# Kernel optimization log

Measured on AMD Instinct MI355X. Metric: run time of the kernel, lower is better.

Reference implementation:

```python
import math
import jax, jax.numpy as jnp
import numpy as np

NUM_HEADS = 12
HEAD_DIM = 64
HIDDEN = NUM_HEADS * HEAD_DIM  # 768
SEQ = 4096


def setup_inputs() -> dict:
    key = jax.random.key(0)
    ks = jax.random.split(key, 7)
    s = 0.02  # BERT-style init scale for weights
    return {
        "hidden_states": jax.random.normal(ks[0], (1, SEQ, HIDDEN), jnp.float32),
        "Wq": jax.random.normal(ks[1], (HIDDEN, HIDDEN), jnp.float32) * s,
        "bq": jax.random.normal(ks[2], (HIDDEN,), jnp.float32) * s,
        "Wk": jax.random.normal(ks[3], (HIDDEN, HIDDEN), jnp.float32) * s,
        "bk": jax.random.normal(ks[4], (HIDDEN,), jnp.float32) * s,
        "Wv": jax.random.normal(ks[5], (HIDDEN, HIDDEN), jnp.float32) * s,
        "bv": jax.random.normal(ks[6], (HIDDEN,), jnp.float32) * s,
    }


def _split_heads(z):
    # [S, HIDDEN] -> [H, S, dh]
    S = z.shape[0]
    return jnp.transpose(z.reshape(S, NUM_HEADS, HEAD_DIM), (1, 0, 2))


def reference(hidden_states, Wq, bq, Wk, bk, Wv, bv):
    # batch is squeezed in the original module (kernel is unbatched)
    x = hidden_states[0]  # [S, D]
    q = _split_heads(x @ Wq.T + bq)  # [H, S, dh]
    k = _split_heads(x @ Wk.T + bk)  # [H, S, dh]
    scale = 1.0 / math.sqrt(HEAD_DIM)
    scores = jnp.einsum('hqd,hkd->hqk', q, k) * scale  # [H, S, S]
    probs = jax.nn.softmax(scores, axis=-1)
    # multi_rand_attn_cuda approximates P @ (x @ Wv^T + bv) via CDF-driven
    # Monte-Carlo column sampling of Wv; its expectation is the exact product,
    # which is the correctness baseline computed here.
    v = _split_heads(x @ Wv.T + bv)  # [H, S, dh]
    ctx = jnp.einsum('hqk,hkd->hqd', probs, v)  # [H, S, dh]
    ctx = jnp.transpose(ctx, (1, 0, 2)).reshape(x.shape[0], HIDDEN)
    return ctx[None]  # [1, S, D]
```

## Files before the change

### kernel.cpp

```cpp
#include <hip/hip_runtime.h>
#include <stdint.h>


typedef float    f32x4 __attribute__((ext_vector_type(4)));
typedef _Float16 h16x8 __attribute__((ext_vector_type(8)));
typedef _Float16 h16x4 __attribute__((ext_vector_type(4)));
typedef _Float16 h16x2 __attribute__((ext_vector_type(2)));
typedef __fp16   fp16x2 __attribute__((ext_vector_type(2)));
typedef unsigned short u16;

#define MFMA32(A, B, C) __builtin_amdgcn_mfma_f32_16x16x32_f16((A), (B), (C), 0, 0, 0)
#define ZERO4 ((f32x4){0.f, 0.f, 0.f, 0.f})

#define SEQ 4096
#define HID 768
#define NH  12
#define DH  64

#define CEXP 0.18033688011112042f

__device__ __forceinline__ u16 f2h(float f) {
  union { _Float16 h; u16 u; } v;
  v.h = (_Float16)f;
  return v.u;
}
__device__ __forceinline__ float h2f(u16 u) {
  union { u16 u; _Float16 h; } v;
  v.u = u;
  return (float)v.h;
}

__device__ __forceinline__ void gload_lds16(const void* g, void* l) {
  __builtin_amdgcn_global_load_lds(
      (__attribute__((address_space(1))) void*)(g),
      (__attribute__((address_space(3))) void*)(l),
      16, 0, 0);
}

__global__ __launch_bounds__(256) void cast_all_k(
    const float* __restrict__ x,  const float* __restrict__ wq,
    const float* __restrict__ wk, const float* __restrict__ wv,
    u16* __restrict__ xh,  u16* __restrict__ wqh,
    u16* __restrict__ wkh, u16* __restrict__ wvh)
{
  int i = blockIdx.x * 256 + threadIdx.x;
  const int NX4 = (SEQ * HID) / 4;
  const int NW4 = (HID * HID) / 4;
  const float4* src; ushort4* dst; int idx;
  if (i < NX4) {
    src = (const float4*)x; dst = (ushort4*)xh; idx = i;
  } else {
    int j = i - NX4;
    int w = j / NW4;
    idx = j - w * NW4;
    src = (const float4*)(w == 0 ? wq : (w == 1 ? wk : wv));
    dst = (ushort4*)(w == 0 ? wqh : (w == 1 ? wkh : wvh));
  }
  float4 v = src[idx];
  ushort4 o;
  o.x = f2h(v.x); o.y = f2h(v.y); o.z = f2h(v.z); o.w = f2h(v.w);
  dst[idx] = o;
}

__global__ __launch_bounds__(256, 3) void qkv_gemm_k(
    const u16* __restrict__ xh,
    const u16* __restrict__ wqh, const u16* __restrict__ wkh, const u16* __restrict__ wvh,
    const float* __restrict__ bq, const float* __restrict__ bk, const float* __restrict__ bv,
    u16* __restrict__ Qh, u16* __restrict__ Kh, u16* __restrict__ Vt)
{
  __shared__ u16 S[128 * 128];

  const int t = threadIdx.x;
  const int wave = t >> 6, lane = t & 63;
  const int m = lane & 15, quad = lane >> 4;
  const int z  = blockIdx.z;
  const int n0 = blockIdx.x * 128;
  const int m0 = blockIdx.y * 128;

  const u16*   W    = (z == 0) ? wqh : (z == 1) ? wkh : wvh;
  const float* bias = (z == 0) ? bq  : (z == 1) ? bk  : bv;

  const int wm = (wave >> 1) * 64;
  const int wn = (wave & 1) * 64;

  f32x4 acc[4][4];
#pragma unroll
  for (int i = 0; i < 4; i++)
#pragma unroll
    for (int j = 0; j < 4; j++) acc[i][j] = ZERO4;

  const int srow = wave * 8 + (lane >> 3);
  const int scg  = (lane & 7) ^ (srow & 7);
  const u16* gA = xh + (m0 + srow) * HID + scg * 8;
  const u16* gB = W  + (n0 + srow) * HID + scg * 8;
  u16* lA = S + wave * 512;
  u16* lB = S + 8192 + wave * 512;

  for (int k0 = 0; k0 < HID; k0 += 64) {
    __syncthreads();
#pragma unroll
    for (int c = 0; c < 4; c++) {
      gload_lds16(gA + c * 32 * HID + k0, lA + c * 2048);
      gload_lds16(gB + c * 32 * HID + k0, lB + c * 2048);
    }
    __syncthreads();

#pragma unroll
    for (int s = 0; s < 2; s++) {
      h16x8 af[4], bf[4];
#pragma unroll
      for (int i = 0; i < 4; i++)
        af[i] = *(const h16x8*)(S + (wm + i * 16 + m) * 64
                                + ((s * 4 + quad) ^ (m & 7)) * 8);
#pragma unroll
      for (int j = 0; j < 4; j++)
        bf[j] = *(const h16x8*)(S + 8192 + (wn + j * 16 + m) * 64
                                + ((s * 4 + quad) ^ (m & 7)) * 8);
#pragma unroll
      for (int i = 0; i < 4; i++)
#pragma unroll
        for (int j = 0; j < 4; j++)
          acc[i][j] = MFMA32(af[i], bf[j], acc[i][j]);
    }
  }

  __syncthreads();

  if (z < 2) {
    const float sc = (z == 0) ? CEXP : 1.0f;
#pragma unroll
    for (int i = 0; i < 4; i++) {
      int sl = wm + i * 16 + quad * 4;
#pragma unroll
      for (int j = 0; j < 4; j++) {
        int colp = wn + j * 16 + m;
        float bb = bias[n0 + colp];
        int c = colp >> 3, sub = colp & 7;
#pragma unroll
        for (int r = 0; r < 4; r++)
          S[(sl + r) * 128 + ((c ^ ((sl + r) & 15)) * 8) + sub] =
              f2h((acc[i][j][r] + bb) * sc);
      }
    }
    __syncthreads();
    u16* outp = (z == 0) ? Qh : Kh;
    const int ch = t & 15;
#pragma unroll
    for (int rr = 0; rr < 8; rr++) {
      int s = rr * 16 + (t >> 4);
      h16x8 v = *(const h16x8*)(S + s * 128 + ((ch ^ (s & 15)) * 8));
      *(h16x8*)(outp + (m0 + s) * HID + n0 + ch * 8) = v;
    }
  } else {
#pragma unroll
    for (int i = 0; i < 4; i++) {
      int sl = wm + i * 16 + quad * 4;
      int vp = (sl & ~31) + ((sl >> 2) & 3) * 8 + ((sl >> 4) & 1) * 4;
#pragma unroll
      for (int j = 0; j < 4; j++) {
        int nl = wn + j * 16 + m;
        float bb = bias[n0 + nl];
        h16x4 o;
        o[0] = (_Float16)(acc[i][j][0] + bb);
        o[1] = (_Float16)(acc[i][j][1] + bb);
        o[2] = (_Float16)(acc[i][j][2] + bb);
        o[3] = (_Float16)(acc[i][j][3] + bb);
        *(h16x4*)(S + nl * 128 + (((vp >> 3) ^ (nl & 15)) * 8) + (vp & 7)) = o;
      }
    }
    __syncthreads();
    const int ch = t & 15;
#pragma unroll
    for (int rr = 0; rr < 8; rr++) {
      int n = rr * 16 + (t >> 4);
      h16x8 v = *(const h16x8*)(S + n * 128 + ((ch ^ (n & 15)) * 8));
      *(h16x8*)(Vt + (n0 + n) * SEQ + m0 + ch * 8) = v;
    }
  }
}

__global__ __launch_bounds__(256, 3) void attn_k(
    const u16* __restrict__ Qh, const u16* __restrict__ Kh, const u16* __restrict__ Vt,
    float* __restrict__ out0, u16* __restrict__ Op1, float* __restrict__ Lp)
{
  __shared__ u16 Ks[128 * 64];
  __shared__ u16 Vs[64 * 128];

  const int t = threadIdx.x;
  const int wave = t >> 6, lane = t & 63;
  const int m = lane & 15, quad = lane >> 4;
  const int h  = blockIdx.y;
  const int q0 = blockIdx.x * 128;
  const int sp = blockIdx.z;
  const int kvbase = sp * 2048;

  h16x8 qf[2][2];
#pragma unroll
  for (int qn = 0; qn < 2; qn++)
#pragma unroll
    for (int ks = 0; ks < 2; ks++)
      qf[qn][ks] = *(const h16x8*)(Qh + (q0 + wave * 32 + qn * 16 + m) * HID
                                   + h * DH + ks * 32 + quad * 8);

  f32x4 O[2][4];
#pragma unroll
  for (int qn = 0; qn < 2; qn++)
#pragma unroll
    for (int jd = 0; jd < 4; jd++) O[qn][jd] = ZERO4;
  float lsum[2] = {0.f, 0.f};

  const int krow_b = wave * 8 + (lane >> 3);
  const int kcl    = lane & 7;
  const int vrow_b = wave * 4 + (lane >> 4);
  const int vcl    = lane & 15;

  for (int it = 0; it < 16; ++it) {
    const int kv0 = kvbase + it * 128;
    __syncthreads();
#pragma unroll
    for (int c = 0; c < 4; c++) {
      int row = c * 32 + krow_b;
      int cg  = kcl ^ (row & 7);
      gload_lds16(Kh + (kv0 + row) * HID + h * DH + cg * 8,
                  Ks + c * 2048 + wave * 512);
      int d  = c * 16 + vrow_b;
      int vg = vcl ^ (d & 15);
      gload_lds16(Vt + (h * DH + d) * SEQ + kv0 + vg * 8,
                  Vs + c * 2048 + wave * 512);
    }
    __syncthreads();

#pragma unroll
    for (int p = 0; p < 4; ++p) {
      const int krow0 = (2 * p) * 16 + m;
      const int krow1 = krow0 + 16;
      h16x8 kb00 = *(const h16x8*)(Ks + krow0 * 64 + ((    quad) ^ (m & 7)) * 8);
      h16x8 kb01 = *(const h16x8*)(Ks + krow0 * 64 + ((4 + quad) ^ (m & 7)) * 8);
      h16x8 kb10 = *(const h16x8*)(Ks + krow1 * 64 + ((    quad) ^ (m & 7)) * 8);
      h16x8 kb11 = *(const h16x8*)(Ks + krow1 * 64 + ((4 + quad) ^ (m & 7)) * 8);

      h16x8 vb[4];
#pragma unroll
      for (int jd = 0; jd < 4; jd++) {
        int d = jd * 16 + m;
        vb[jd] = *(const h16x8*)(Vs + d * 128 + (((p * 4 + quad) ^ m) * 8));
      }

#pragma unroll
      for (int qn = 0; qn < 2; qn++) {
        f32x4 S0 = MFMA32(kb00, qf[qn][0], ZERO4);
        S0       = MFMA32(kb01, qf[qn][1], S0);
        f32x4 S1 = MFMA32(kb10, qf[qn][0], ZERO4);
        S1       = MFMA32(kb11, qf[qn][1], S1);

        float e0 = __builtin_amdgcn_exp2f(S0[0]);
        float e1 = __builtin_amdgcn_exp2f(S0[1]);
        float e2 = __builtin_amdgcn_exp2f(S0[2]);
        float e3 = __builtin_amdgcn_exp2f(S0[3]);
        float e4 = __builtin_amdgcn_exp2f(S1[0]);
        float e5 = __builtin_amdgcn_exp2f(S1[1]);
        float e6 = __builtin_amdgcn_exp2f(S1[2]);
        float e7 = __builtin_amdgcn_exp2f(S1[3]);
        lsum[qn] += ((e0 + e1) + (e2 + e3)) + ((e4 + e5) + (e6 + e7));

        fp16x2 p01 = __builtin_amdgcn_cvt_pkrtz(e0, e1);
        fp16x2 p23 = __builtin_amdgcn_cvt_pkrtz(e2, e3);
        fp16x2 p45 = __builtin_amdgcn_cvt_pkrtz(e4, e5);
        fp16x2 p67 = __builtin_amdgcn_cvt_pkrtz(e6, e7);
        h16x2 q01 = __builtin_bit_cast(h16x2, p01);
        h16x2 q23 = __builtin_bit_cast(h16x2, p23);
        h16x2 q45 = __builtin_bit_cast(h16x2, p45);
        h16x2 q67 = __builtin_bit_cast(h16x2, p67);
        h16x4 pl = __builtin_shufflevector(q01, q23, 0, 1, 2, 3);
        h16x4 ph = __builtin_shufflevector(q45, q67, 0, 1, 2, 3);
        h16x8 pa = __builtin_shufflevector(pl, ph, 0, 1, 2, 3, 4, 5, 6, 7);

#pragma unroll
        for (int jd = 0; jd < 4; jd++)
          O[qn][jd] = MFMA32(pa, vb[jd], O[qn][jd]);
      }
    }
  }

#pragma unroll
  for (int qn = 0; qn < 2; qn++) {
    float v = lsum[qn];
    v += __shfl_xor(v, 16, 64);
    v += __shfl_xor(v, 32, 64);
    if (quad == 0)
      Lp[sp * NH * SEQ + h * SEQ + q0 + wave * 32 + qn * 16 + m] = v;
#pragma unroll
    for (int jd = 0; jd < 4; jd++) {
      int col = h * DH + jd * 16 + m;
#pragma unroll
      for (int r = 0; r < 4; r++) {
        int row = q0 + wave * 32 + qn * 16 + quad * 4 + r;
        if (sp == 0) out0[row * HID + col] = O[qn][jd][r];
        else         Op1[row * HID + col] = f2h(O[qn][jd][r]);
      }
    }
  }
}

__global__ __launch_bounds__(256) void reduce_k(
    float* __restrict__ out, const u16* __restrict__ Op1,
    const float* __restrict__ Lp)
{
  int i = blockIdx.x * 256 + threadIdx.x;
  int s  = i / 192;
  int c4 = i - s * 192;
  int h  = c4 >> 4;
  float L = Lp[h * SEQ + s] + Lp[NH * SEQ + h * SEQ + s];
  float inv = __builtin_amdgcn_rcpf(L);
  float4 a = ((const float4*)out)[i];
  ushort4 b = ((const ushort4*)Op1)[i];
  float4 r;
  r.x = (a.x + h2f(b.x)) * inv;
  r.y = (a.y + h2f(b.y)) * inv;
  r.z = (a.z + h2f(b.z)) * inv;
  r.w = (a.w + h2f(b.w)) * inv;
  ((float4*)out)[i] = r;
}

extern "C" void kernel_launch(void* const* d_in, const int* in_sizes, int n_in,
                              void* d_out, int out_size, void* d_ws, size_t ws_size,
                              hipStream_t stream) {
  const float* x  = (const float*)d_in[0];
  const float* Wq = (const float*)d_in[1];
  const float* bq = (const float*)d_in[2];
  const float* Wk = (const float*)d_in[3];
  const float* bk = (const float*)d_in[4];
  const float* Wv = (const float*)d_in[5];
  const float* bv = (const float*)d_in[6];
  float* out = (float*)d_out;

  char* ws = (char*)d_ws;
  u16* Qh  = (u16*)(ws);
  u16* Kh  = (u16*)(ws + 6291456);
  u16* Vt  = (u16*)(ws + 12582912);
  u16* xh  = (u16*)(ws + 18874368);
  u16* wqh = (u16*)(ws + 25165824);
  u16* wkh = (u16*)(ws + 26345472);
  u16* wvh = (u16*)(ws + 27525120);
  u16*   Op1 = (u16*)(ws + 18874368);
  float* Lp  = (float*)(ws + 25165824);

  cast_all_k<<<4800, 256, 0, stream>>>(x, Wq, Wk, Wv, xh, wqh, wkh, wvh);
  qkv_gemm_k<<<dim3(6, 32, 3), 256, 0, stream>>>(xh, wqh, wkh, wvh,
                                                 bq, bk, bv, Qh, Kh, Vt);
  attn_k<<<dim3(32, NH, 2), 256, 0, stream>>>(Qh, Kh, Vt, out, Op1, Lp);
  reduce_k<<<3072, 256, 0, stream>>>(out, Op1, Lp);
}
```

Baseline: 160.6 us.

## Double-buffer K/V tiles in attention and compute row sums via MFMA

Changes the attention inner loop from single-buffered 128-key tiles with two syncthreads per iteration to double-buffered 64-key tiles. The next tile's global-to-LDS load is issued before computing on the current one, with explicit vmcnt waits and raw barriers. The softmax denominator is now computed with an extra MFMA against a ones vector instead of VALU adds and shuffles, and MFMA sections get raised wave priority. This aims to hide load latency and cut VALU work, at the cost of an extra MFMA per step and hand-managed waitcnt correctness.

New measurement: 159.2 us. About the same (-0.8%).

```diff
diff --git a/kernel.cpp b/kernel.cpp
--- a/kernel.cpp
+++ b/kernel.cpp
@@ -18,6 +18,8 @@
 #define DH  64
 
 #define CEXP 0.18033688011112042f
+
+#define WAITV(N) asm volatile("s_waitcnt vmcnt(" #N ")" ::: "memory")
 
 __device__ __forceinline__ u16 f2h(float f) {
   union { _Float16 h; u16 u; } v;
@@ -179,12 +181,84 @@
   }
 }
 
+
+__device__ __forceinline__ void stage_kv(const u16* gKb, const u16* gVb,
+                                         u16* lK, u16* lV, int kv0)
+{
+#pragma unroll
+  for (int c = 0; c < 2; c++) {
+    gload_lds16(gKb + (kv0 + c * 32) * HID, lK + c * 2048);
+    gload_lds16(gVb + c * 32 * SEQ + kv0,   lV + c * 2048);
+  }
+}
+
+__device__ __forceinline__ void attn_compute(
+    const u16* __restrict__ Kb, const u16* __restrict__ Vb,
+    const h16x8 (&qf)[2][2], f32x4 (&O)[2][4], f32x4 (&Lacc)[2],
+    h16x8 onesv, int m, int quad)
+{
+#pragma unroll
+  for (int p = 0; p < 2; ++p) {
+    const int krow0 = 32 * p + m;
+    const int krow1 = krow0 + 16;
+    h16x8 kb00 = *(const h16x8*)(Kb + krow0 * 64 + ((    quad) ^ (m & 7)) * 8);
+    h16x8 kb01 = *(const h16x8*)(Kb + krow0 * 64 + ((4 + quad) ^ (m & 7)) * 8);
+    h16x8 kb10 = *(const h16x8*)(Kb + krow1 * 64 + ((    quad) ^ (m & 7)) * 8);
+    h16x8 kb11 = *(const h16x8*)(Kb + krow1 * 64 + ((4 + quad) ^ (m & 7)) * 8);
+
+    h16x8 vb[4];
+#pragma unroll
+    for (int jd = 0; jd < 4; jd++) {
+      int d = jd * 16 + m;
+      vb[jd] = *(const h16x8*)(Vb + d * 64 + (((p * 4 + quad) ^ (m & 7)) * 8));
+    }
+
+#pragma unroll
+    for (int qn = 0; qn < 2; qn++) {
+      __builtin_amdgcn_s_setprio(1);
+      f32x4 S0 = MFMA32(kb00, qf[qn][0], ZERO4);
+      S0       = MFMA32(kb01, qf[qn][1], S0);
+      f32x4 S1 = MFMA32(kb10, qf[qn][0], ZERO4);
+      S1       = MFMA32(kb11, qf[qn][1], S1);
+      __builtin_amdgcn_s_setprio(0);
+
+      float e0 = __builtin_amdgcn_exp2f(S0[0]);
+      float e1 = __builtin_amdgcn_exp2f(S0[1]);
+      float e2 = __builtin_amdgcn_exp2f(S0[2]);
+      float e3 = __builtin_amdgcn_exp2f(S0[3]);
+      float e4 = __builtin_amdgcn_exp2f(S1[0]);
+      float e5 = __builtin_amdgcn_exp2f(S1[1]);
+      float e6 = __builtin_amdgcn_exp2f(S1[2]);
+      float e7 = __builtin_amdgcn_exp2f(S1[3]);
+
+      fp16x2 p01 = __builtin_amdgcn_cvt_pkrtz(e0, e1);
+      fp16x2 p23 = __builtin_amdgcn_cvt_pkrtz(e2, e3);
+      fp16x2 p45 = __builtin_amdgcn_cvt_pkrtz(e4, e5);
+      fp16x2 p67 = __builtin_amdgcn_cvt_pkrtz(e6, e7);
+      h16x2 q01 = __builtin_bit_cast(h16x2, p01);
+      h16x2 q23 = __builtin_bit_cast(h16x2, p23);
+      h16x2 q45 = __builtin_bit_cast(h16x2, p45);
+      h16x2 q67 = __builtin_bit_cast(h16x2, p67);
+      h16x4 pl = __builtin_shufflevector(q01, q23, 0, 1, 2, 3);
+      h16x4 ph = __builtin_shufflevector(q45, q67, 0, 1, 2, 3);
+      h16x8 pa = __builtin_shufflevector(pl, ph, 0, 1, 2, 3, 4, 5, 6, 7);
+
+      __builtin_amdgcn_s_setprio(1);
+#pragma unroll
+      for (int jd = 0; jd < 4; jd++)
+        O[qn][jd] = MFMA32(pa, vb[jd], O[qn][jd]);
+      Lacc[qn] = MFMA32(pa, onesv, Lacc[qn]);
+      __builtin_amdgcn_s_setprio(0);
+    }
+  }
+}
+
 __global__ __launch_bounds__(256, 3) void attn_k(
     const u16* __restrict__ Qh, const u16* __restrict__ Kh, const u16* __restrict__ Vt,
     float* __restrict__ out0, u16* __restrict__ Op1, float* __restrict__ Lp)
 {
-  __shared__ u16 Ks[128 * 64];
-  __shared__ u16 Vs[64 * 128];
+  __shared__ u16 Ks[2][64 * 64];
+  __shared__ u16 Vs[2][64 * 64];
 
   const int t = threadIdx.x;
   const int wave = t >> 6, lane = t & 63;
@@ -207,88 +281,53 @@
   for (int qn = 0; qn < 2; qn++)
 #pragma unroll
     for (int jd = 0; jd < 4; jd++) O[qn][jd] = ZERO4;
-  float lsum[2] = {0.f, 0.f};
-
-  const int krow_b = wave * 8 + (lane >> 3);
-  const int kcl    = lane & 7;
-  const int vrow_b = wave * 4 + (lane >> 4);
-  const int vcl    = lane & 15;
-
-  for (int it = 0; it < 16; ++it) {
-    const int kv0 = kvbase + it * 128;
-    __syncthreads();
-#pragma unroll
-    for (int c = 0; c < 4; c++) {
-      int row = c * 32 + krow_b;
-      int cg  = kcl ^ (row & 7);
-      gload_lds16(Kh + (kv0 + row) * HID + h * DH + cg * 8,
-                  Ks + c * 2048 + wave * 512);
-      int d  = c * 16 + vrow_b;
-      int vg = vcl ^ (d & 15);
-      gload_lds16(Vt + (h * DH + d) * SEQ + kv0 + vg * 8,
-                  Vs + c * 2048 + wave * 512);
-    }
-    __syncthreads();
-
-#pragma unroll
-    for (int p = 0; p < 4; ++p) {
-      const int krow0 = (2 * p) * 16 + m;
-      const int krow1 = krow0 + 16;
-      h16x8 kb00 = *(const h16x8*)(Ks + krow0 * 64 + ((    quad) ^ (m & 7)) * 8);
-      h16x8 kb01 = *(const h16x8*)(Ks + krow0 * 64 + ((4 + quad) ^ (m & 7)) * 8);
-      h16x8 kb10 = *(const h16x8*)(Ks + krow1 * 64 + ((    quad) ^ (m & 7)) * 8);
-      h16x8 kb11 = *(const h16x8*)(Ks + krow1 * 64 + ((4 + quad) ^ (m & 7)) * 8);
-
-      h16x8 vb[4];
-#pragma unroll
-      for (int jd = 0; jd < 4; jd++) {
-        int d = jd * 16 + m;
-        vb[jd] = *(const h16x8*)(Vs + d * 128 + (((p * 4 + quad) ^ m) * 8));
-      }
-
-#pragma unroll
-      for (int qn = 0; qn < 2; qn++) {
-        f32x4 S0 = MFMA32(kb00, qf[qn][0], ZERO4);
-        S0       = MFMA32(kb01, qf[qn][1], S0);
-        f32x4 S1 = MFMA32(kb10, qf[qn][0], ZERO4);
-        S1       = MFMA32(kb11, qf[qn][1], S1);
-
-        float e0 = __builtin_amdgcn_exp2f(S0[0]);
-        float e1 = __builtin_amdgcn_exp2f(S0[1]);
-        float e2 = __builtin_amdgcn_exp2f(S0[2]);
-        float e3 = __builtin_amdgcn_exp2f(S0[3]);
-        float e4 = __builtin_amdgcn_exp2f(S1[0]);
-        float e5 = __builtin_amdgcn_exp2f(S1[1]);
-        float e6 = __builtin_amdgcn_exp2f(S1[2]);
-        float e7 = __builtin_amdgcn_exp2f(S1[3]);
-        lsum[qn] += ((e0 + e1) + (e2 + e3)) + ((e4 + e5) + (e6 + e7));
-
-        fp16x2 p01 = __builtin_amdgcn_cvt_pkrtz(e0, e1);
-        fp16x2 p23 = __builtin_amdgcn_cvt_pkrtz(e2, e3);
-        fp16x2 p45 = __builtin_amdgcn_cvt_pkrtz(e4, e5);
-        fp16x2 p67 = __builtin_amdgcn_cvt_pkrtz(e6, e7);
-        h16x2 q01 = __builtin_bit_cast(h16x2, p01);
-        h16x2 q23 = __builtin_bit_cast(h16x2, p23);
-        h16x2 q45 = __builtin_bit_cast(h16x2, p45);
-        h16x2 q67 = __builtin_bit_cast(h16x2, p67);
-        h16x4 pl = __builtin_shufflevector(q01, q23, 0, 1, 2, 3);
-        h16x4 ph = __builtin_shufflevector(q45, q67, 0, 1, 2, 3);
-        h16x8 pa = __builtin_shufflevector(pl, ph, 0, 1, 2, 3, 4, 5, 6, 7);
-
-#pragma unroll
-        for (int jd = 0; jd < 4; jd++)
-          O[qn][jd] = MFMA32(pa, vb[jd], O[qn][jd]);
-      }
-    }
+  f32x4 Lacc[2] = {ZERO4, ZERO4};
+
+  h16x8 onesv;
+#pragma unroll
+  for (int j = 0; j < 8; j++) onesv[j] = (_Float16)1.0f;
+
+  const int srow = wave * 8 + (lane >> 3);
+  const int swz  = ((lane & 7) ^ (srow & 7)) * 8;
+  const u16* gKb = Kh + srow * HID + h * DH + swz;
+  const u16* gVb = Vt + (h * DH + srow) * SEQ + swz;
+  u16* lK0 = &Ks[0][wave * 512];
+  u16* lK1 = &Ks[1][wave * 512];
+  u16* lV0 = &Vs[0][wave * 512];
+  u16* lV1 = &Vs[1][wave * 512];
+
+  stage_kv(gKb, gVb, lK0, lV0, kvbase);
+
+  for (int it = 0; it < 32; it += 2) {
+    stage_kv(gKb, gVb, lK1, lV1, kvbase + (it + 1) * 64);
+    WAITV(4);
+    __builtin_amdgcn_s_barrier();
+    __builtin_amdgcn_sched_barrier(0);
+    attn_compute(&Ks[0][0], &Vs[0][0], qf, O, Lacc, onesv, m, quad);
+    __builtin_amdgcn_s_barrier();
+    __builtin_amdgcn_sched_barrier(0);
+
+    if (it + 2 < 32) {
+      stage_kv(gKb, gVb, lK0, lV0, kvbase + (it + 2) * 64);
+      WAITV(4);
+    } else {
+      WAITV(0);
+    }
+    __builtin_amdgcn_s_barrier();
+    __builtin_amdgcn_sched_barrier(0);
+    attn_compute(&Ks[1][0], &Vs[1][0], qf, O, Lacc, onesv, m, quad);
+    __builtin_amdgcn_s_barrier();
+    __builtin_amdgcn_sched_barrier(0);
   }
 
 #pragma unroll
   for (int qn = 0; qn < 2; qn++) {
-    float v = lsum[qn];
-    v += __shfl_xor(v, 16, 64);
-    v += __shfl_xor(v, 32, 64);
-    if (quad == 0)
-      Lp[sp * NH * SEQ + h * SEQ + q0 + wave * 32 + qn * 16 + m] = v;
+    if (m == 0) {
+#pragma unroll
+      for (int r = 0; r < 4; r++)
+        Lp[sp * NH * SEQ + h * SEQ + q0 + wave * 32 + qn * 16 + quad * 4 + r] =
+            Lacc[qn][r];
+    }
 #pragma unroll
     for (int jd = 0; jd < 4; jd++) {
       int col = h * DH + jd * 16 + m;
```
